# Kernel optimization log

Hardware: AMD Instinct MI355X
Metric: run time of the kernel (lower is better)

The kernel has to match this reference:

```python
import jax, jax.numpy as jnp
import numpy as np

B, S, D = 8, 2048, 1024
PADDING_IDX = 0
NEG_BIG = -1000000000.0


def setup_inputs() -> dict:
    key = jax.random.key(0)
    k1, k2, k3 = jax.random.split(key, 3)
    state = jax.random.normal(k1, (B, S, D), dtype=jnp.float32)
    x = jax.random.normal(k2, (B, S, D), dtype=jnp.float32)
    src = jax.random.randint(k3, (B, S), 0, 5, dtype=jnp.int64)
    return {"state": state, "x": x, "src": src}


def reference(state, x, src):
    # mask: True at padding positions, shape [B, S]
    mask = src == PADDING_IDX
    # scores[b,s,t] = <state[b,s], x[b,t]>
    scores = jnp.einsum("bsd,btd->bst", state, x)
    scores = jnp.where(mask[:, :, None], NEG_BIG, scores)
    # softmax over the source (s) axis, dim=-2
    p_attn = jax.nn.softmax(scores, axis=-2)  # [B, S, T]
    # w = (state^T @ p_attn)^T -> [B, T, D]
    w = jnp.einsum("bsd,bst->btd", state, p_attn)
    # in-place mask: rows at padding positions set to -inf (T == S here)
    w = jnp.where(mask[:, :, None], -jnp.inf, w)
    attn_score = jax.nn.softmax(w, axis=1)  # softmax over T per feature
    # out = (state^T @ attn_score)^T -> [B, D, D]
    out = jnp.einsum("bsd,bse->bed", state, attn_score)
    return out
```

## Files before the change

kernel.cpp:

```cpp
#include <hip/hip_runtime.h>
#include <hip/hip_bf16.h>

#define SS 2048
#define TT 2048
#define DD 1024
#define NB 8

typedef __attribute__((ext_vector_type(8))) short short8v;
typedef __attribute__((ext_vector_type(8))) unsigned short us8;
typedef __attribute__((ext_vector_type(4))) unsigned short us4;
typedef __attribute__((ext_vector_type(4))) float f32x4;

__device__ __forceinline__ float bf2f(unsigned short u) {
    union { unsigned int i; float f; } v; v.i = ((unsigned int)u) << 16; return v.f;
}
__device__ __forceinline__ unsigned short f2bf(float f) {
    union { float f; unsigned int i; } v; v.f = f;
    unsigned int x = v.i;
    return (unsigned short)((x + 0x7fffu + ((x >> 16) & 1u)) >> 16);
}

__global__ __launch_bounds__(256) void conv_k(
    const float* __restrict__ in, unsigned short* __restrict__ outv, size_t n)
{
    size_t i = ((size_t)blockIdx.x * 256 + threadIdx.x) * 8;
    const size_t stride = (size_t)gridDim.x * 256 * 8;
    for (; i < n; i += stride) {
        float4 a = *reinterpret_cast<const float4*>(in + i);
        float4 b = *reinterpret_cast<const float4*>(in + i + 4);
        us8 o;
        o[0] = f2bf(a.x); o[1] = f2bf(a.y); o[2] = f2bf(a.z); o[3] = f2bf(a.w);
        o[4] = f2bf(b.x); o[5] = f2bf(b.y); o[6] = f2bf(b.z); o[7] = f2bf(b.w);
        *reinterpret_cast<us8*>(outv + i) = o;
    }
}

__global__ __launch_bounds__(256) void transpose_k(
    const float* __restrict__ in, unsigned short* __restrict__ outT,
    unsigned short* __restrict__ outB, size_t sIn, size_t sOutT, size_t sOutB)
{
    __shared__ float t[64][65];
    const int g = blockIdx.z;
    const float* I = in + g * sIn;
    unsigned short* OT = outT + g * sOutT;
    unsigned short* OB = outB + g * sOutB;
    const int s0 = blockIdx.x * 64, d0 = blockIdx.y * 64;
    const int tid = threadIdx.x;
    #pragma unroll
    for (int i = 0; i < 4; ++i) {
        int slot = tid + i * 256;
        int rr = slot >> 4, rc = (slot & 15) * 4;
        float4 v = *reinterpret_cast<const float4*>(I + (size_t)(s0 + rr) * DD + d0 + rc);
        t[rr][rc + 0] = v.x; t[rr][rc + 1] = v.y; t[rr][rc + 2] = v.z; t[rr][rc + 3] = v.w;
        us4 o; o[0] = f2bf(v.x); o[1] = f2bf(v.y); o[2] = f2bf(v.z); o[3] = f2bf(v.w);
        *reinterpret_cast<us4*>(OB + (size_t)(s0 + rr) * DD + d0 + rc) = o;
    }
    __syncthreads();
    #pragma unroll
    for (int i = 0; i < 4; ++i) {
        int slot = tid + i * 256;
        int dr = slot >> 4, sidx = (slot & 15) * 4;
        us4 o;
        #pragma unroll
        for (int j = 0; j < 4; ++j) o[j] = f2bf(t[sidx + j][dr]);
        *reinterpret_cast<us4*>(OT + (size_t)(d0 + dr) * SS + s0 + sidx) = o;
    }
}

template<int OUT_F32>
__global__ __launch_bounds__(256, 4) void gemm_nt(
    const unsigned short* __restrict__ A, const unsigned short* __restrict__ B,
    void* __restrict__ C, int lda, int ldb, int ldc, int K,
    size_t sA, size_t sB, size_t sC)
{
    __shared__ unsigned short As[2][128 * 32];
    __shared__ unsigned short Bs[2][128 * 32];

    const int nxy = gridDim.x * gridDim.y;
    const int nwg = nxy * gridDim.z;
    int wg = blockIdx.x + gridDim.x * (blockIdx.y + gridDim.y * blockIdx.z);
    if ((nwg & 7) == 0) {
        const int cpx = nwg >> 3;
        wg = (wg & 7) * cpx + (wg >> 3);
    }
    const int g  = wg / nxy;
    const int rm = wg - g * nxy;
    const int by = rm / gridDim.x;
    const int bx = rm - by * gridDim.x;

    const unsigned short* Ag = A + g * sA;
    const unsigned short* Bg = B + g * sB;
    const int m0 = by * 128, n0 = bx * 128;
    const int tid = threadIdx.x, lane = tid & 63, wid = tid >> 6;
    const int wm = (wid >> 1) * 64, wn = (wid & 1) * 64;
    const int lr16 = lane & 15, lk = lane >> 4;
    const int sr = wid * 32 + (lane >> 2);
    const int sp = lane & 3;

    f32x4 acc[4][4] = {};
    const int NT = K >> 5;

#define STAGE(buf, kt)                                                          \
    {                                                                           \
        const int k0 = (kt) << 5;                                               \
        _Pragma("unroll")                                                       \
        for (int j = 0; j < 2; ++j) {                                           \
            int r = sr + j * 16;                                                \
            int c = sp ^ ((r >> 1) & 3);                                        \
            __builtin_amdgcn_global_load_lds(                                   \
                (const __attribute__((address_space(1))) unsigned int*)        \
                    (Ag + (size_t)(m0 + r) * lda + k0 + c * 8),                 \
                (__attribute__((address_space(3))) unsigned int*)              \
                    (&As[buf][(wid * 32 + j * 16) * 32]),                       \
                16, 0, 0);                                                      \
            __builtin_amdgcn_global_load_lds(                                   \
                (const __attribute__((address_space(1))) unsigned int*)        \
                    (Bg + (size_t)(n0 + r) * ldb + k0 + c * 8),                 \
                (__attribute__((address_space(3))) unsigned int*)              \
                    (&Bs[buf][(wid * 32 + j * 16) * 32]),                       \
                16, 0, 0);                                                      \
        }                                                                       \
    }

    int cur = 0;
    STAGE(0, 0);
    __syncthreads();
    for (int kt = 0; kt < NT; ++kt) {
        if (kt + 1 < NT) STAGE(cur ^ 1, kt + 1);
        short8v a[4], bb[4];
        #pragma unroll
        for (int mi = 0; mi < 4; ++mi) {
            int r = wm + mi * 16 + lr16;
            a[mi] = *reinterpret_cast<const short8v*>(
                &As[cur][r * 32 + (lk ^ ((r >> 1) & 3)) * 8]);
        }
        #pragma unroll
        for (int ni = 0; ni < 4; ++ni) {
            int r = wn + ni * 16 + lr16;
            bb[ni] = *reinterpret_cast<const short8v*>(
                &Bs[cur][r * 32 + (lk ^ ((r >> 1) & 3)) * 8]);
        }
        #pragma unroll
        for (int ni = 0; ni < 4; ++ni)
            #pragma unroll
            for (int mi = 0; mi < 4; ++mi)
                acc[mi][ni] = __builtin_amdgcn_mfma_f32_16x16x32_bf16(a[mi], bb[ni], acc[mi][ni], 0, 0, 0);
        __syncthreads();
        cur ^= 1;
    }
#undef STAGE

    const int orow = (lane >> 4) * 4, ocol = lane & 15;
    if (OUT_F32) {
        float* Cg = (float*)C + g * sC;
        #pragma unroll
        for (int mi = 0; mi < 4; ++mi)
            #pragma unroll
            for (int ni = 0; ni < 4; ++ni)
                #pragma unroll
                for (int r = 0; r < 4; ++r)
                    Cg[(size_t)(m0 + wm + mi * 16 + orow + r) * ldc + (n0 + wn + ni * 16 + ocol)] = acc[mi][ni][r];
    } else {
        unsigned short* Cg = (unsigned short*)C + g * sC;
        #pragma unroll
        for (int mi = 0; mi < 4; ++mi)
            #pragma unroll
            for (int ni = 0; ni < 4; ++ni)
                #pragma unroll
                for (int r = 0; r < 4; ++r)
                    Cg[(size_t)(m0 + wm + mi * 16 + orow + r) * ldc + (n0 + wn + ni * 16 + ocol)] = f2bf(acc[mi][ni][r]);
    }
}

__global__ __launch_bounds__(256) void softmax1_k(
    unsigned short* __restrict__ P, const float* __restrict__ x,
    const float* __restrict__ state, const int* __restrict__ src,
    int b0, size_t sP)
{
    const int t = blockIdx.x, g = blockIdx.y, b = b0 + g, tid = threadIdx.x;
    const int lane = tid & 63, wid = tid >> 6;
    unsigned short* row = P + g * sP + (size_t)t * SS;
    const int* sb = src + (size_t)b * SS;
    __shared__ float redA[4], redB[4];
    __shared__ int cnt, list[96];
    __shared__ float corr[96];

    us8 rv = *reinterpret_cast<const us8*>(row + tid * 8);
    int4 mk0 = reinterpret_cast<const int4*>(sb)[tid * 2];
    int4 mk1 = reinterpret_cast<const int4*>(sb)[tid * 2 + 1];
    int msk[8] = { mk0.x == 0, mk0.y == 0, mk0.z == 0, mk0.w == 0,
                   mk1.x == 0, mk1.y == 0, mk1.z == 0, mk1.w == 0 };
    float v[8];
    float m = -1e30f;
    #pragma unroll
    for (int i = 0; i < 8; ++i) {
        v[i] = msk[i] ? -1e30f : bf2f(rv[i]);
        m = fmaxf(m, v[i]);
    }
    #pragma unroll
    for (int o = 32; o > 0; o >>= 1) m = fmaxf(m, __shfl_xor(m, o, 64));
    if (lane == 0) redA[wid] = m;
    if (tid == 0) cnt = 0;
    __syncthreads();
    const float M = fmaxf(fmaxf(redA[0], redA[1]), fmaxf(redA[2], redA[3]));
    #pragma unroll
    for (int i = 0; i < 8; ++i) {
        if (!msk[i] && v[i] > M - 16.f) {
            int j = atomicAdd(&cnt, 1);
            if (j < 96) list[j] = tid * 8 + i;
        }
    }
    __syncthreads();
    const int n = min(cnt, 96);
    const float* xr = x + (size_t)b * SS * DD + (size_t)t * DD;
    float4 xa[4];
    #pragma unroll
    for (int c = 0; c < 4; ++c) xa[c] = reinterpret_cast<const float4*>(xr)[lane + c * 64];
    for (int j = wid; j < n; j += 4) {
        const float* sr = state + (size_t)b * SS * DD + (size_t)list[j] * DD;
        float p = 0.f;
        #pragma unroll
        for (int c = 0; c < 4; ++c) {
            float4 c4 = reinterpret_cast<const float4*>(sr)[lane + c * 64];
            p += xa[c].x * c4.x + xa[c].y * c4.y + xa[c].z * c4.z + xa[c].w * c4.w;
        }
        #pragma unroll
        for (int o = 32; o > 0; o >>= 1) p += __shfl_xor(p, o, 64);
        if (lane == 0) corr[j] = p;
    }
    __syncthreads();
    for (int j = 0; j < n; ++j) {
        int s = list[j];
        if ((s >> 3) == tid) v[s & 7] = corr[j];
    }
    float m2 = -1e30f;
    #pragma unroll
    for (int i = 0; i < 8; ++i) m2 = fmaxf(m2, v[i]);
    #pragma unroll
    for (int o = 32; o > 0; o >>= 1) m2 = fmaxf(m2, __shfl_xor(m2, o, 64));
    if (lane == 0) redA[wid] = m2;
    __syncthreads();
    const float M2 = fmaxf(fmaxf(redA[0], redA[1]), fmaxf(redA[2], redA[3]));
    float l = 0.f;
    #pragma unroll
    for (int i = 0; i < 8; ++i) if (!msk[i]) { v[i] = __expf(v[i] - M2); l += v[i]; }
    #pragma unroll
    for (int o = 32; o > 0; o >>= 1) l += __shfl_xor(l, o, 64);
    if (lane == 0) redB[wid] = l;
    __syncthreads();
    const float inv = 1.f / (redB[0] + redB[1] + redB[2] + redB[3]);
    us8 ov;
    #pragma unroll
    for (int i = 0; i < 8; ++i) ov[i] = msk[i] ? 0 : f2bf(v[i] * inv);
    *reinterpret_cast<us8*>(row + tid * 8) = ov;
}

__global__ __launch_bounds__(256) void softmax2_k(
    const unsigned short* __restrict__ wT, unsigned short* __restrict__ attnT,
    const int* __restrict__ src, int b0, size_t sW, size_t sAt)
{
    const int e = blockIdx.x, g = blockIdx.y, b = b0 + g, tid = threadIdx.x;
    const int lane = tid & 63, wid = tid >> 6;
    const unsigned short* row = wT + g * sW + (size_t)e * TT;
    unsigned short* orow = attnT + g * sAt + (size_t)e * TT;
    const int* sb = src + (size_t)b * SS;
    __shared__ float shm[4], shl[4];
    us8 rv = *reinterpret_cast<const us8*>(row + tid * 8);
    int4 mk0 = reinterpret_cast<const int4*>(sb)[tid * 2];
    int4 mk1 = reinterpret_cast<const int4*>(sb)[tid * 2 + 1];
    int msk[8] = { mk0.x == 0, mk0.y == 0, mk0.z == 0, mk0.w == 0,
                   mk1.x == 0, mk1.y == 0, mk1.z == 0, mk1.w == 0 };
    float v[8];
    float m = -1e30f;
    #pragma unroll
    for (int i = 0; i < 8; ++i) {
        v[i] = msk[i] ? -1e30f : bf2f(rv[i]);
        m = fmaxf(m, v[i]);
    }
    #pragma unroll
    for (int o = 32; o > 0; o >>= 1) m = fmaxf(m, __shfl_xor(m, o, 64));
    if (lane == 0) shm[wid] = m;
    __syncthreads();
    const float M = fmaxf(fmaxf(shm[0], shm[1]), fmaxf(shm[2], shm[3]));
    float l = 0.f;
    #pragma unroll
    for (int i = 0; i < 8; ++i) if (!msk[i]) { v[i] = __expf(v[i] - M); l += v[i]; }
    #pragma unroll
    for (int o = 32; o > 0; o >>= 1) l += __shfl_xor(l, o, 64);
    if (lane == 0) shl[wid] = l;
    __syncthreads();
    const float inv = 1.f / (shl[0] + shl[1] + shl[2] + shl[3]);
    us8 ov;
    #pragma unroll
    for (int i = 0; i < 8; ++i) ov[i] = msk[i] ? 0 : f2bf(v[i] * inv);
    *reinterpret_cast<us8*>(orow + tid * 8) = ov;
}

extern "C" void kernel_launch(void* const* d_in, const int* in_sizes, int n_in,
                              void* d_out, int out_size, void* d_ws, size_t ws_size,
                              hipStream_t stream)
{
    const float* state = (const float*)d_in[0];
    const float* x     = (const float*)d_in[1];
    const int* src     = (const int*)d_in[2];
    float* out         = (float*)d_out;

    const size_t SD = (size_t)SS * DD;
    const size_t perP  = (size_t)SS * TT * 2;
    const size_t perST = (size_t)DD * SS * 2;
    const size_t perW  = (size_t)DD * TT * 2;
    const size_t perXB = (size_t)SS * DD * 2;
    const size_t perSB = (size_t)SS * DD * 2;
    const size_t perBatch = perP + perST + perW + perXB + perSB;

    int G = 8;
    while (G > 1 && (size_t)G * perBatch > ws_size) G >>= 1;

    char* base = (char*)d_ws;
    unsigned short* P  = (unsigned short*)base;
    unsigned short* ST = (unsigned short*)(base + (size_t)G * perP);
    unsigned short* W  = (unsigned short*)(base + (size_t)G * (perP + perST));
    unsigned short* XB = (unsigned short*)(base + (size_t)G * (perP + perST + perW));
    unsigned short* SB = (unsigned short*)(base + (size_t)G * (perP + perST + perW + perXB));

    const size_t sP  = (size_t)SS * TT;
    const size_t sST = (size_t)DD * SS;
    const size_t sW  = (size_t)DD * TT;
    const size_t sXB = (size_t)SS * DD;

    for (int b0 = 0; b0 < NB; b0 += G) {
        conv_k<<<2048, 256, 0, stream>>>(x + (size_t)b0 * SD, XB, (size_t)G * SD);
        transpose_k<<<dim3(SS / 64, DD / 64, G), 256, 0, stream>>>(
            state + (size_t)b0 * SD, ST, SB, SD, sST, sXB);

        gemm_nt<0><<<dim3(SS / 128, TT / 128, G), 256, 0, stream>>>(
            XB, SB, P, DD, DD, SS, DD, sXB, sXB, sP);

        softmax1_k<<<dim3(TT, G), 256, 0, stream>>>(P, x, state, src, b0, sP);

        gemm_nt<0><<<dim3(TT / 128, DD / 128, G), 256, 0, stream>>>(
            ST, P, W, SS, SS, TT, SS, sST, sP, sW);

        softmax2_k<<<dim3(DD, G), 256, 0, stream>>>(W, P, src, b0, sW, sP);

        gemm_nt<1><<<dim3(DD / 128, DD / 128, G), 256, 0, stream>>>(
            P, ST, out + (size_t)b0 * DD * DD, TT, SS, DD, TT, sP, sST, (size_t)DD * DD);
    }
}
```

Baseline: 337.9 us.

## Add 256x256 tiled bf16 GEMM kernel for the two large GEMMs

Adds a gemm256 kernel with 512 threads, 256x256 output tiles, a K-step of 64, double-buffered direct global-to-LDS loads and XOR swizzling. It replaces the 128x128 gemm_nt for the scores GEMM and the W GEMM. Larger tiles give more data reuse per LDS load and fewer global reads. In exchange it uses 128KB of LDS per block and 128 accumulator registers per thread, which lowers occupancy. The grid for the W GEMM also shrinks (8x4xG), which risks leaving compute units idle.

```diff
diff --git a/kernel.cpp b/kernel.cpp
--- a/kernel.cpp
+++ b/kernel.cpp
@@ -64,6 +64,120 @@
         #pragma unroll
         for (int j = 0; j < 4; ++j) o[j] = f2bf(t[sidx + j][dr]);
         *reinterpret_cast<us4*>(OT + (size_t)(d0 + dr) * SS + s0 + sidx) = o;
+    }
+}
+
+template<int OUT_F32>
+__global__ __launch_bounds__(512, 2) void gemm256(
+    const unsigned short* __restrict__ A, const unsigned short* __restrict__ B,
+    void* __restrict__ C, int lda, int ldb, int ldc, int K,
+    size_t sA, size_t sB, size_t sC)
+{
+    __shared__ unsigned short As[2][256 * 64];
+    __shared__ unsigned short Bs[2][256 * 64];
+
+    const int nxy = gridDim.x * gridDim.y;
+    const int nwg = nxy * gridDim.z;
+    int wg = blockIdx.x + gridDim.x * (blockIdx.y + gridDim.y * blockIdx.z);
+    if ((nwg & 7) == 0) {
+        const int cpx = nwg >> 3;
+        wg = (wg & 7) * cpx + (wg >> 3);
+    }
+    const int g  = wg / nxy;
+    const int rm = wg - g * nxy;
+    const int by = rm / gridDim.x;
+    const int bx = rm - by * gridDim.x;
+
+    const unsigned short* Ag = A + g * sA;
+    const unsigned short* Bg = B + g * sB;
+    const int m0 = by * 256, n0 = bx * 256;
+    const int tid = threadIdx.x, lane = tid & 63, wid = tid >> 6;
+    const int wr = wid >> 2, wc = wid & 3;
+    const int lr = lane & 15, lkc = lane >> 4;
+    const int strow = tid >> 3;
+    const int stsp = tid & 7;
+
+    f32x4 acc[8][4] = {};
+    const int NT = K >> 6;
+
+#define STAGE256(buf, kt)                                                       \
+    {                                                                           \
+        const int k0 = (kt) << 6;                                               \
+        _Pragma("unroll")                                                       \
+        for (int j = 0; j < 4; ++j) {                                           \
+            int r = j * 64 + strow;                                             \
+            int c = stsp ^ (r & 7);                                             \
+            __builtin_amdgcn_global_load_lds(                                   \
+                (const __attribute__((address_space(1))) unsigned int*)        \
+                    (Ag + (size_t)(m0 + r) * lda + k0 + c * 8),                 \
+                (__attribute__((address_space(3))) unsigned int*)              \
+                    (&As[buf][j * 4096 + wid * 512]),                           \
+                16, 0, 0);                                                      \
+        }                                                                       \
+        _Pragma("unroll")                                                       \
+        for (int j = 0; j < 4; ++j) {                                           \
+            int r = j * 64 + strow;                                             \
+            int c = stsp ^ (r & 7);                                             \
+            __builtin_amdgcn_global_load_lds(                                   \
+                (const __attribute__((address_space(1))) unsigned int*)        \
+                    (Bg + (size_t)(n0 + r) * ldb + k0 + c * 8),                 \
+                (__attribute__((address_space(3))) unsigned int*)              \
+                    (&Bs[buf][j * 4096 + wid * 512]),                           \
+                16, 0, 0);                                                      \
+        }                                                                       \
+    }
+
+    int cur = 0;
+    STAGE256(0, 0);
+    __syncthreads();
+    for (int kt = 0; kt < NT; ++kt) {
+        if (kt + 1 < NT) STAGE256(cur ^ 1, kt + 1);
+        #pragma unroll
+        for (int ksub = 0; ksub < 2; ++ksub) {
+            const int c0 = ksub * 4 + lkc;
+            short8v a[8], bb[4];
+            #pragma unroll
+            for (int mi = 0; mi < 8; ++mi) {
+                int r = wr * 128 + mi * 16 + lr;
+                a[mi] = *reinterpret_cast<const short8v*>(
+                    &As[cur][r * 64 + ((c0 ^ (r & 7)) * 8)]);
+            }
+            #pragma unroll
+            for (int ni = 0; ni < 4; ++ni) {
+                int r = wc * 64 + ni * 16 + lr;
+                bb[ni] = *reinterpret_cast<const short8v*>(
+                    &Bs[cur][r * 64 + ((c0 ^ (r & 7)) * 8)]);
+            }
+            #pragma unroll
+            for (int ni = 0; ni < 4; ++ni)
+                #pragma unroll
+                for (int mi = 0; mi < 8; ++mi)
+                    acc[mi][ni] = __builtin_amdgcn_mfma_f32_16x16x32_bf16(a[mi], bb[ni], acc[mi][ni], 0, 0, 0);
+        }
+        __syncthreads();
+        cur ^= 1;
+    }
+#undef STAGE256
+
+    const int orow = (lane >> 4) * 4, ocol = lane & 15;
+    if (OUT_F32) {
+        float* Cg = (float*)C + g * sC;
+        #pragma unroll
+        for (int mi = 0; mi < 8; ++mi)
+            #pragma unroll
+            for (int ni = 0; ni < 4; ++ni)
+                #pragma unroll
+                for (int r = 0; r < 4; ++r)
+                    Cg[(size_t)(m0 + wr * 128 + mi * 16 + orow + r) * ldc + (n0 + wc * 64 + ni * 16 + ocol)] = acc[mi][ni][r];
+    } else {
+        unsigned short* Cg = (unsigned short*)C + g * sC;
+        #pragma unroll
+        for (int mi = 0; mi < 8; ++mi)
+            #pragma unroll
+            for (int ni = 0; ni < 4; ++ni)
+                #pragma unroll
+                for (int r = 0; r < 4; ++r)
+                    Cg[(size_t)(m0 + wr * 128 + mi * 16 + orow + r) * ldc + (n0 + wc * 64 + ni * 16 + ocol)] = f2bf(acc[mi][ni][r]);
     }
 }
 
@@ -333,12 +447,12 @@
         transpose_k<<<dim3(SS / 64, DD / 64, G), 256, 0, stream>>>(
             state + (size_t)b0 * SD, ST, SB, SD, sST, sXB);
 
-        gemm_nt<0><<<dim3(SS / 128, TT / 128, G), 256, 0, stream>>>(
+        gemm256<0><<<dim3(SS / 256, TT / 256, G), 512, 0, stream>>>(
             XB, SB, P, DD, DD, SS, DD, sXB, sXB, sP);
 
         softmax1_k<<<dim3(TT, G), 256, 0, stream>>>(P, x, state, src, b0, sP);
 
-        gemm_nt<0><<<dim3(TT / 128, DD / 128, G), 256, 0, stream>>>(
+        gemm256<0><<<dim3(TT / 256, DD / 256, G), 512, 0, stream>>>(
             ST, P, W, SS, SS, TT, SS, sST, sP, sW);
 
         softmax2_k<<<dim3(DD, G), 256, 0, stream>>>(W, P, src, b0, sW, sP);
```

Result: faster. 328.7 us (-2.7%).
